# Performance work log

Measured on AMD Instinct MI355X. Metric: run time of the kernel, lower is better.

The kernel has to match this reference:

```python
import jax, jax.numpy as jnp
import numpy as np

B, L, D, C = 16, 1444, 128, 21  # batch, graph_len (38*38), feature dim, num_classes


def setup_inputs() -> dict:
    key = jax.random.key(0)
    k1, k2, k3 = jax.random.split(key, 3)
    cls_r_prob = jax.random.uniform(k1, (C, C), dtype=jnp.float32)
    source = jax.random.normal(k2, (B, L, D), dtype=jnp.float32)
    class_idx = jax.random.randint(k3, (B, L), 0, C, dtype=jnp.int64)
    return {"cls_r_prob": cls_r_prob, "source": source, "class_idx": class_idx}


def reference(cls_r_prob, source, class_idx):
    # Vectorized build_local_graph:
    # torch loop sets graph[n,i,j] = P[ci, cj] for j < i, then adds its transpose
    # and an identity whose diagonal is zeroed where class_idx == 0.
    G = cls_r_prob[class_idx[:, :, None], class_idx[:, None, :]]  # [B, L, L] pairwise gather
    M = jnp.tril(G, -1)                                           # strict lower triangle
    graph = M + jnp.swapaxes(M, 1, 2)                             # symmetrize
    ar = jnp.arange(L)
    diag = (class_idx != 0).astype(source.dtype)                  # [B, L]
    graph = graph.at[:, ar, ar].add(diag)                         # masked identity
    # bmm aggregation: fused_buffer = graph @ source
    fused = jnp.einsum('bij,bjd->bid', graph, source)             # [B, L, D]
    return fused, source
```

## Files before the change

### kernel.cpp

```cpp
#include <hip/hip_runtime.h>
#include <hip/hip_bf16.h>

#define BB 16
#define LL 1444
#define DD 128
#define CC 21
#define CH 38
#define NK 38

#define CS_ELEMS ((size_t)BB*NK*CC*DD)
#define TOT_ELEMS ((size_t)BB*CC*DD)

__global__ __launch_bounds__(128) void k1_chunk_sums(
    const float* __restrict__ src, const int* __restrict__ idx,
    float* __restrict__ cs, float* __restrict__ src_copy)
{
  int blk = blockIdx.x;
  int b = blk / NK, k = blk % NK;
  int d = threadIdx.x;
  int i0 = k * CH;
  float acc[CC];
#pragma unroll
  for (int c = 0; c < CC; ++c) acc[c] = 0.f;
  const int* idxb = idx + b * LL;
  for (int t = 0; t < CH; ++t) {
    int i = i0 + t;
    int ci = idxb[i];
    size_t off = ((size_t)(b * LL + i)) * DD + d;
    float v = src[off];
    src_copy[off] = v;
#pragma unroll
    for (int c = 0; c < CC; ++c) acc[c] += (ci == c) ? v : 0.f;
  }
  float* o = cs + ((size_t)(b * NK + k)) * CC * DD + d;
#pragma unroll
  for (int c = 0; c < CC; ++c) o[c * DD] = acc[c];
}

__global__ __launch_bounds__(128) void k2_scan(
    float* __restrict__ cs, float* __restrict__ tot)
{
  int b = blockIdx.x / CC, c = blockIdx.x % CC;
  int d = threadIdx.x;
  float run = 0.f;
  for (int k = 0; k < NK; ++k) {
    size_t off = (((size_t)(b * NK + k)) * CC + c) * DD + d;
    float t = cs[off];
    cs[off] = run;
    run += t;
  }
  tot[((size_t)(b * CC + c)) * DD + d] = run;
}

__global__ __launch_bounds__(128) void k3_R(
    const float* __restrict__ P, const float* __restrict__ tot,
    float* __restrict__ R)
{
  int b = blockIdx.x / CC, a = blockIdx.x % CC;
  int d = threadIdx.x;
  float r = 0.f;
#pragma unroll
  for (int c = 0; c < CC; ++c)
    r += P[c * CC + a] * tot[((size_t)(b * CC + c)) * DD + d];
  R[((size_t)(b * CC + a)) * DD + d] = r;
}

__global__ __launch_bounds__(128) void k4_fused(
    const float* __restrict__ src, const int* __restrict__ idx,
    const float* __restrict__ P, const float* __restrict__ cs,
    const float* __restrict__ R, float* __restrict__ out)
{
  __shared__ float Qs[CC * CC];
  __shared__ float Ss[CC];
  int b = blockIdx.x / NK, k = blockIdx.x % NK;
  int d = threadIdx.x;

  for (int t = threadIdx.x; t < CC * CC; t += blockDim.x) {
    int a = t / CC, c = t % CC;
    Qs[t] = P[a * CC + c] - P[c * CC + a];
  }
  if (threadIdx.x < CC) {
    int a = threadIdx.x;
    Ss[a] = (a != 0 ? 1.0f : 0.0f) - P[a * CC + a];
  }
  __syncthreads();

  float pre[CC];
  const float* csb = cs + ((size_t)(b * NK + k)) * CC * DD + d;
#pragma unroll
  for (int c = 0; c < CC; ++c) pre[c] = csb[c * DD];

  int i0 = k * CH;
  const int* idxb = idx + b * LL;
  for (int t = 0; t < CH; ++t) {
    int i = i0 + t;
    int ci = idxb[i];
    size_t off = ((size_t)(b * LL + i)) * DD + d;
    float v = src[off];
    float acc = R[((size_t)(b * CC + ci)) * DD + d] + Ss[ci] * v;
    const float* q = &Qs[ci * CC];
#pragma unroll
    for (int c = 0; c < CC; ++c) acc += q[c] * pre[c];
    out[off] = acc;
#pragma unroll
    for (int c = 0; c < CC; ++c) pre[c] += (ci == c) ? v : 0.f;
  }
}

extern "C" void kernel_launch(void* const* d_in, const int* in_sizes, int n_in,
                              void* d_out, int out_size, void* d_ws, size_t ws_size,
                              hipStream_t stream) {
  const float* P   = (const float*)d_in[0];
  const float* src = (const float*)d_in[1];
  const int*   idx = (const int*)d_in[2];

  float* out_fused = (float*)d_out;
  float* out_src   = out_fused + (size_t)BB * LL * DD;

  float* cs  = (float*)d_ws;
  float* tot = cs + CS_ELEMS;
  float* R   = tot + TOT_ELEMS;

  k1_chunk_sums<<<BB * NK, 128, 0, stream>>>(src, idx, cs, out_src);
  k2_scan<<<BB * CC, 128, 0, stream>>>(cs, tot);
  k3_R<<<BB * CC, 128, 0, stream>>>(P, tot, R);
  k4_fused<<<BB * NK, 128, 0, stream>>>(src, idx, P, cs, R, out_fused);
}
```

Before: 116.9 us.

## Fuse R computation into main kernel, halve chunk size, batch loads, use scalar lanes

Removes the separate k3_R launch by having each k4 block recompute the 21x128 R tile from per-class totals and keep it in shared memory. Chunk length drops from 38 to 19 rows, doubling the number of blocks so more CUs are busy. All source rows for a chunk are loaded into registers up front, and class indices are read from shared memory and made wave-uniform with readfirstlane. Q coefficients are fetched with readlane, so the class selects become scalar branches. In exchange, every k4 block redoes the 21x21 R matrix product, the scan in k2 is longer, and register pressure rises.

```diff
diff --git a/kernel.cpp b/kernel.cpp
--- a/kernel.cpp
+++ b/kernel.cpp
@@ -5,8 +5,8 @@
 #define LL 1444
 #define DD 128
 #define CC 21
-#define CH 38
-#define NK 38
+#define CH 19
+#define NK 76
 
 #define CS_ELEMS ((size_t)BB*NK*CC*DD)
 #define TOT_ELEMS ((size_t)BB*CC*DD)
@@ -15,26 +15,37 @@
     const float* __restrict__ src, const int* __restrict__ idx,
     float* __restrict__ cs, float* __restrict__ src_copy)
 {
-  int blk = blockIdx.x;
-  int b = blk / NK, k = blk % NK;
+  __shared__ int cidx[CH];
+  int b = blockIdx.x / NK, k = blockIdx.x % NK;
   int d = threadIdx.x;
   int i0 = k * CH;
+  if (threadIdx.x < CH) cidx[threadIdx.x] = idx[b * LL + i0 + threadIdx.x];
+  __syncthreads();
+
+  const float* s0 = src + ((size_t)(b * LL + i0)) * DD + d;
+  float v[CH];
+#pragma unroll
+  for (int t = 0; t < CH; ++t) v[t] = s0[(size_t)t * DD];
+
+  float* c0 = src_copy + ((size_t)(b * LL + i0)) * DD + d;
+#pragma unroll
+  for (int t = 0; t < CH; ++t) c0[(size_t)t * DD] = v[t];
+
   float acc[CC];
 #pragma unroll
   for (int c = 0; c < CC; ++c) acc[c] = 0.f;
-  const int* idxb = idx + b * LL;
+
+#pragma unroll
   for (int t = 0; t < CH; ++t) {
-    int i = i0 + t;
-    int ci = idxb[i];
-    size_t off = ((size_t)(b * LL + i)) * DD + d;
-    float v = src[off];
-    src_copy[off] = v;
+    int sci = __builtin_amdgcn_readfirstlane(cidx[t]);
 #pragma unroll
-    for (int c = 0; c < CC; ++c) acc[c] += (ci == c) ? v : 0.f;
+    for (int c = 0; c < CC; ++c)
+      if (sci == c) acc[c] += v[t];
   }
+
   float* o = cs + ((size_t)(b * NK + k)) * CC * DD + d;
 #pragma unroll
-  for (int c = 0; c < CC; ++c) o[c * DD] = acc[c];
+  for (int c = 0; c < CC; ++c) o[(size_t)c * DD] = acc[c];
 }
 
 __global__ __launch_bounds__(128) void k2_scan(
@@ -42,40 +53,35 @@
 {
   int b = blockIdx.x / CC, c = blockIdx.x % CC;
   int d = threadIdx.x;
+  float* base = cs + ((size_t)b * NK * CC + c) * DD + d;
+  float vals[NK];
+#pragma unroll
+  for (int k = 0; k < NK; ++k) vals[k] = base[(size_t)k * CC * DD];
   float run = 0.f;
+#pragma unroll
   for (int k = 0; k < NK; ++k) {
-    size_t off = (((size_t)(b * NK + k)) * CC + c) * DD + d;
-    float t = cs[off];
-    cs[off] = run;
+    float t = vals[k];
+    base[(size_t)k * CC * DD] = run;
     run += t;
   }
   tot[((size_t)(b * CC + c)) * DD + d] = run;
 }
 
-__global__ __launch_bounds__(128) void k3_R(
-    const float* __restrict__ P, const float* __restrict__ tot,
-    float* __restrict__ R)
-{
-  int b = blockIdx.x / CC, a = blockIdx.x % CC;
-  int d = threadIdx.x;
-  float r = 0.f;
-#pragma unroll
-  for (int c = 0; c < CC; ++c)
-    r += P[c * CC + a] * tot[((size_t)(b * CC + c)) * DD + d];
-  R[((size_t)(b * CC + a)) * DD + d] = r;
-}
-
 __global__ __launch_bounds__(128) void k4_fused(
     const float* __restrict__ src, const int* __restrict__ idx,
     const float* __restrict__ P, const float* __restrict__ cs,
-    const float* __restrict__ R, float* __restrict__ out)
+    const float* __restrict__ tot, float* __restrict__ out)
 {
   __shared__ float Qs[CC * CC];
   __shared__ float Ss[CC];
+  __shared__ float Rl[CC][DD];
+  __shared__ int cidx[CH];
+
   int b = blockIdx.x / NK, k = blockIdx.x % NK;
   int d = threadIdx.x;
+  int i0 = k * CH;
 
-  for (int t = threadIdx.x; t < CC * CC; t += blockDim.x) {
+  for (int t = threadIdx.x; t < CC * CC; t += 128) {
     int a = t / CC, c = t % CC;
     Qs[t] = P[a * CC + c] - P[c * CC + a];
   }
@@ -83,27 +89,50 @@
     int a = threadIdx.x;
     Ss[a] = (a != 0 ? 1.0f : 0.0f) - P[a * CC + a];
   }
-  __syncthreads();
+  if (threadIdx.x < CH) cidx[threadIdx.x] = idx[b * LL + i0 + threadIdx.x];
+
+  float tt[CC];
+#pragma unroll
+  for (int c = 0; c < CC; ++c) tt[c] = tot[((size_t)(b * CC + c)) * DD + d];
+#pragma unroll
+  for (int a = 0; a < CC; ++a) {
+    float r = 0.f;
+#pragma unroll
+    for (int c = 0; c < CC; ++c) r += P[c * CC + a] * tt[c];
+    Rl[a][d] = r;
+  }
 
   float pre[CC];
   const float* csb = cs + ((size_t)(b * NK + k)) * CC * DD + d;
 #pragma unroll
-  for (int c = 0; c < CC; ++c) pre[c] = csb[c * DD];
+  for (int c = 0; c < CC; ++c) pre[c] = csb[(size_t)c * DD];
 
-  int i0 = k * CH;
-  const int* idxb = idx + b * LL;
+  const float* s0 = src + ((size_t)(b * LL + i0)) * DD + d;
+  float v[CH];
+#pragma unroll
+  for (int t = 0; t < CH; ++t) v[t] = s0[(size_t)t * DD];
+
+  __syncthreads();
+
+  int lane = threadIdx.x & 63;
+  float qcol[CC];
+#pragma unroll
+  for (int c = 0; c < CC; ++c) qcol[c] = (lane < CC) ? Qs[lane * CC + c] : 0.f;
+
+  float* o0 = out + ((size_t)(b * LL + i0)) * DD + d;
+#pragma unroll
   for (int t = 0; t < CH; ++t) {
-    int i = i0 + t;
-    int ci = idxb[i];
-    size_t off = ((size_t)(b * LL + i)) * DD + d;
-    float v = src[off];
-    float acc = R[((size_t)(b * CC + ci)) * DD + d] + Ss[ci] * v;
-    const float* q = &Qs[ci * CC];
+    int sci = __builtin_amdgcn_readfirstlane(cidx[t]);
+    float acc = Rl[sci][d] + Ss[sci] * v[t];
 #pragma unroll
-    for (int c = 0; c < CC; ++c) acc += q[c] * pre[c];
-    out[off] = acc;
+    for (int c = 0; c < CC; ++c) {
+      float q = __uint_as_float(__builtin_amdgcn_readlane(__float_as_uint(qcol[c]), sci));
+      acc += q * pre[c];
+    }
+    o0[(size_t)t * DD] = acc;
 #pragma unroll
-    for (int c = 0; c < CC; ++c) pre[c] += (ci == c) ? v : 0.f;
+    for (int c = 0; c < CC; ++c)
+      if (sci == c) pre[c] += v[t];
   }
 }
 
@@ -119,10 +148,8 @@
 
   float* cs  = (float*)d_ws;
   float* tot = cs + CS_ELEMS;
-  float* R   = tot + TOT_ELEMS;
 
   k1_chunk_sums<<<BB * NK, 128, 0, stream>>>(src, idx, cs, out_src);
   k2_scan<<<BB * CC, 128, 0, stream>>>(cs, tot);
-  k3_R<<<BB * CC, 128, 0, stream>>>(P, tot, R);
-  k4_fused<<<BB * NK, 128, 0, stream>>>(src, idx, P, cs, R, out_fused);
+  k4_fused<<<BB * NK, 128, 0, stream>>>(src, idx, P, cs, tot, out_fused);
 }
```

New measurement: 125.0 us. +7.0%, slower.

## Recast chunk output as small GEMM over LDS-staged inputs and drop R kernel

Applied to the files above, without the earlier changes.

The per-chunk sequential prefix update becomes a small dense matrix product. Each block builds a coefficient matrix G in shared memory covering the intra-chunk lower triangle, the antisymmetric prefix term and the P-transpose times total term. Source rows, prefix sums and totals are staged into LDS with global_load_lds, and each wave computes 19 rows. This removes the k3_R launch and the serial dependency chain, and also stages k1 through LDS with 256 threads, split class accumulators and float4 copies. k2 batches its loads into registers. The cost is more FLOPs (a dense triangle) and larger shared memory per block, which may lower occupancy.

```diff
diff --git a/kernel.cpp b/kernel.cpp
--- a/kernel.cpp
+++ b/kernel.cpp
@@ -1,5 +1,4 @@
 #include <hip/hip_runtime.h>
-#include <hip/hip_bf16.h>
 
 #define BB 16
 #define LL 1444
@@ -7,34 +6,61 @@
 #define CC 21
 #define CH 38
 #define NK 38
+#define RH 19
+#define KK (CH + 2*CC)
 
 #define CS_ELEMS ((size_t)BB*NK*CC*DD)
-#define TOT_ELEMS ((size_t)BB*CC*DD)
 
-__global__ __launch_bounds__(128) void k1_chunk_sums(
+#define ASG __attribute__((address_space(1)))
+#define ASL __attribute__((address_space(3)))
+
+static __device__ __forceinline__ void gll16(const float* g, float* l) {
+  __builtin_amdgcn_global_load_lds((const ASG void*)g, (ASL void*)l, 16, 0, 0);
+}
+static __device__ __forceinline__ void gll4(const float* g, float* l) {
+  __builtin_amdgcn_global_load_lds((const ASG void*)g, (ASL void*)l, 4, 0, 0);
+}
+
+__global__ __launch_bounds__(256) void k1_chunk_sums(
     const float* __restrict__ src, const int* __restrict__ idx,
     float* __restrict__ cs, float* __restrict__ src_copy)
 {
-  int blk = blockIdx.x;
-  int b = blk / NK, k = blk % NK;
-  int d = threadIdx.x;
-  int i0 = k * CH;
-  float acc[CC];
+  __shared__ __align__(16) float Vs[CH][DD];
+  int tid = threadIdx.x;
+  int w = tid >> 6, lane = tid & 63;
+  int b = blockIdx.x / NK, kc = blockIdx.x % NK;
+  int i0 = kc * CH;
+  const float* sc = src + (size_t)(b * LL + i0) * DD;
+
+  for (int i = w; i < 19; i += 4)
+    gll16(sc + i * 256 + lane * 4, &Vs[0][0] + i * 256);
+  __syncthreads();
+
+  const int* gidx = idx + b * LL + i0;
+  int d = tid & 127;
+  int c0 = (tid >> 7) * 10;
+  float acc[11];
 #pragma unroll
-  for (int c = 0; c < CC; ++c) acc[c] = 0.f;
-  const int* idxb = idx + b * LL;
+  for (int j = 0; j < 11; ++j) acc[j] = 0.f;
+
+#pragma unroll
   for (int t = 0; t < CH; ++t) {
-    int i = i0 + t;
-    int ci = idxb[i];
-    size_t off = ((size_t)(b * LL + i)) * DD + d;
-    float v = src[off];
-    src_copy[off] = v;
+    int ct = gidx[t];
+    float v = Vs[t][d];
 #pragma unroll
-    for (int c = 0; c < CC; ++c) acc[c] += (ci == c) ? v : 0.f;
+    for (int j = 0; j < 11; ++j) {
+      float m = (ct == c0 + j) ? 1.0f : 0.0f;
+      acc[j] += m * v;
+    }
   }
-  float* o = cs + ((size_t)(b * NK + k)) * CC * DD + d;
+
+  float* co = cs + ((size_t)(b * NK + kc) * CC) * DD + d;
 #pragma unroll
-  for (int c = 0; c < CC; ++c) o[c * DD] = acc[c];
+  for (int j = 0; j < 11; ++j) co[(c0 + j) * DD] = acc[j];
+
+  const float4* v4 = (const float4*)&Vs[0][0];
+  float4* o4 = (float4*)(src_copy + (size_t)(b * LL + i0) * DD);
+  for (int i = tid; i < CH * DD / 4; i += 256) o4[i] = v4[i];
 }
 
 __global__ __launch_bounds__(128) void k2_scan(
@@ -42,69 +68,98 @@
 {
   int b = blockIdx.x / CC, c = blockIdx.x % CC;
   int d = threadIdx.x;
+  float* base = cs + ((size_t)(b * NK) * CC + c) * DD + d;
+  const int S = CC * DD;
+  float a[RH];
   float run = 0.f;
-  for (int k = 0; k < NK; ++k) {
-    size_t off = (((size_t)(b * NK + k)) * CC + c) * DD + d;
-    float t = cs[off];
-    cs[off] = run;
-    run += t;
-  }
+#pragma unroll
+  for (int i = 0; i < RH; ++i) a[i] = base[(size_t)i * S];
+#pragma unroll
+  for (int i = 0; i < RH; ++i) { float t = a[i]; base[(size_t)i * S] = run; run += t; }
+#pragma unroll
+  for (int i = 0; i < RH; ++i) a[i] = base[(size_t)(RH + i) * S];
+#pragma unroll
+  for (int i = 0; i < RH; ++i) { float t = a[i]; base[(size_t)(RH + i) * S] = run; run += t; }
   tot[((size_t)(b * CC + c)) * DD + d] = run;
 }
 
-__global__ __launch_bounds__(128) void k3_R(
-    const float* __restrict__ P, const float* __restrict__ tot,
-    float* __restrict__ R)
-{
-  int b = blockIdx.x / CC, a = blockIdx.x % CC;
-  int d = threadIdx.x;
-  float r = 0.f;
-#pragma unroll
-  for (int c = 0; c < CC; ++c)
-    r += P[c * CC + a] * tot[((size_t)(b * CC + c)) * DD + d];
-  R[((size_t)(b * CC + a)) * DD + d] = r;
-}
+#define GEMM_BODY(kv)                                                   \
+  {                                                                     \
+    float x = X[(kv)][d];                                               \
+    const float4* gp = (const float4*)(Gh + (kv) * 20);                 \
+    float4 g0 = gp[0], g1 = gp[1], g2 = gp[2], g3 = gp[3], g4 = gp[4];  \
+    acc[0]  += g0.x * x; acc[1]  += g0.y * x; acc[2]  += g0.z * x;      \
+    acc[3]  += g0.w * x; acc[4]  += g1.x * x; acc[5]  += g1.y * x;      \
+    acc[6]  += g1.z * x; acc[7]  += g1.w * x; acc[8]  += g2.x * x;      \
+    acc[9]  += g2.y * x; acc[10] += g2.z * x; acc[11] += g2.w * x;      \
+    acc[12] += g3.x * x; acc[13] += g3.y * x; acc[14] += g3.z * x;      \
+    acc[15] += g3.w * x; acc[16] += g4.x * x; acc[17] += g4.y * x;      \
+    acc[18] += g4.z * x;                                                \
+  }
 
-__global__ __launch_bounds__(128) void k4_fused(
+__global__ __launch_bounds__(256) void k4_fused(
     const float* __restrict__ src, const int* __restrict__ idx,
     const float* __restrict__ P, const float* __restrict__ cs,
-    const float* __restrict__ R, float* __restrict__ out)
+    const float* __restrict__ tot, float* __restrict__ out)
 {
-  __shared__ float Qs[CC * CC];
-  __shared__ float Ss[CC];
-  int b = blockIdx.x / NK, k = blockIdx.x % NK;
-  int d = threadIdx.x;
+  __shared__ __align__(16) float X[KK][DD];
+  __shared__ __align__(16) float GA[KK][20];
+  __shared__ __align__(16) float GB[KK][20];
 
-  for (int t = threadIdx.x; t < CC * CC; t += blockDim.x) {
-    int a = t / CC, c = t % CC;
-    Qs[t] = P[a * CC + c] - P[c * CC + a];
-  }
-  if (threadIdx.x < CC) {
-    int a = threadIdx.x;
-    Ss[a] = (a != 0 ? 1.0f : 0.0f) - P[a * CC + a];
+  int tid = threadIdx.x;
+  int w = tid >> 6, lane = tid & 63;
+  int b = blockIdx.x / NK, kc = blockIdx.x % NK;
+  int i0 = kc * CH;
+
+  const float* sc = src + (size_t)(b * LL + i0) * DD;
+  const float* pc = cs + ((size_t)(b * NK + kc) * CC) * DD;
+  const float* tb = tot + (size_t)b * CC * DD;
+  float* xf = &X[0][0];
+
+  for (int i = w; i < 19; i += 4) gll16(sc + i * 256 + lane * 4, xf + i * 256);
+  for (int i = w; i < 10; i += 4) gll16(pc + i * 256 + lane * 4, xf + CH * DD + i * 256);
+  for (int i = w; i < 10; i += 4) gll16(tb + i * 256 + lane * 4, xf + (CH + CC) * DD + i * 256);
+  if (w < 2) gll4(pc + 2560 + w * 64 + lane, xf + CH * DD + 2560 + w * 64);
+  else       gll4(tb + 2560 + (w - 2) * 64 + lane, xf + (CH + CC) * DD + 2560 + (w - 2) * 64);
+
+  const int* gidx = idx + b * LL + i0;
+  for (int e = tid; e < 2 * KK * 20; e += 256) {
+    int h = e / (KK * 20);
+    int rem = e - h * (KK * 20);
+    int k = rem / 20, j = rem - k * 20;
+    int t = h * RH + j;
+    float val = 0.f;
+    if (j < RH) {
+      int ct = gidx[t];
+      if (k < CH) {
+        if (k < t) { int ck = gidx[k]; val = P[ct * CC + ck] - P[ck * CC + ct]; }
+        else if (k == t) val = (ct != 0 ? 1.0f : 0.0f) - P[ct * CC + ct];
+      } else if (k < CH + CC) {
+        int c = k - CH; val = P[ct * CC + c] - P[c * CC + ct];
+      } else {
+        int c = k - CH - CC; val = P[c * CC + ct];
+      }
+    }
+    (h ? &GB[0][0] : &GA[0][0])[k * 20 + j] = val;
   }
   __syncthreads();
 
-  float pre[CC];
-  const float* csb = cs + ((size_t)(b * NK + k)) * CC * DD + d;
+  int rw = __builtin_amdgcn_readfirstlane(w >> 1);
+  int dh = w & 1;
+  int d = dh * 64 + lane;
+  const float* Gh = rw ? &GB[0][0] : &GA[0][0];
+
+  float acc[RH];
 #pragma unroll
-  for (int c = 0; c < CC; ++c) pre[c] = csb[c * DD];
+  for (int j = 0; j < RH; ++j) acc[j] = 0.f;
 
-  int i0 = k * CH;
-  const int* idxb = idx + b * LL;
-  for (int t = 0; t < CH; ++t) {
-    int i = i0 + t;
-    int ci = idxb[i];
-    size_t off = ((size_t)(b * LL + i)) * DD + d;
-    float v = src[off];
-    float acc = R[((size_t)(b * CC + ci)) * DD + d] + Ss[ci] * v;
-    const float* q = &Qs[ci * CC];
+  int kend1 = __builtin_amdgcn_readfirstlane(rw ? CH : RH);
+  for (int k = 0; k < kend1; ++k) GEMM_BODY(k)
+  for (int k = CH; k < KK; ++k)   GEMM_BODY(k)
+
+  float* op = out + (size_t)(b * LL + i0 + rw * RH) * DD + d;
 #pragma unroll
-    for (int c = 0; c < CC; ++c) acc += q[c] * pre[c];
-    out[off] = acc;
-#pragma unroll
-    for (int c = 0; c < CC; ++c) pre[c] += (ci == c) ? v : 0.f;
-  }
+  for (int j = 0; j < RH; ++j) op[(size_t)j * DD] = acc[j];
 }
 
 extern "C" void kernel_launch(void* const* d_in, const int* in_sizes, int n_in,
@@ -119,10 +174,8 @@
 
   float* cs  = (float*)d_ws;
   float* tot = cs + CS_ELEMS;
-  float* R   = tot + TOT_ELEMS;
 
-  k1_chunk_sums<<<BB * NK, 128, 0, stream>>>(src, idx, cs, out_src);
+  k1_chunk_sums<<<BB * NK, 256, 0, stream>>>(src, idx, cs, out_src);
   k2_scan<<<BB * CC, 128, 0, stream>>>(cs, tot);
-  k3_R<<<BB * CC, 128, 0, stream>>>(P, tot, R);
-  k4_fused<<<BB * NK, 128, 0, stream>>>(src, idx, P, cs, R, out_fused);
+  k4_fused<<<BB * NK, 256, 0, stream>>>(src, idx, P, cs, tot, out_fused);
 }
```

After: 102.2 us (median of 2 runs). 1.14x faster.
